# Performance work log

Hardware: AMD Instinct MI355X
Metric: run time of the kernel (lower is better)

Reference implementation:

```python
import jax, jax.numpy as jnp
import numpy as np

DECAY_CONSTANT = 1.0  # init kwarg decay_constant


def setup_inputs() -> dict:
    key = jax.random.key(0)
    k1, k2 = jax.random.split(key)
    B, E, S = 8, 1024, 2048
    x = jax.random.normal(k1, (B, E, S), dtype=jnp.float32)
    weight = jax.random.normal(k2, (1, S), dtype=jnp.float32)
    bias = jnp.zeros((S,), dtype=jnp.float32)
    decay_value = jnp.ones((1,), dtype=jnp.float32)
    return {"x": x, "weight": weight, "bias": bias, "decay_value": decay_value}


def _vector_to_matrix(v, decay_value):
    # v: (S,). M[i, j] = v[j] * clip(decay, 0.9, 1)^((j - i)/c) for j >= i, else 0.
    S = v.shape[0]
    i = jnp.arange(S)[:, None]
    j = jnp.arange(S)[None, :]
    d = jnp.clip(decay_value, 0.9, 1.0)  # shape (1,), broadcasts
    expo = (j - i).astype(v.dtype) / jnp.asarray(DECAY_CONSTANT, v.dtype)
    M = jnp.where(j >= i, v[None, :] * (d ** expo), jnp.zeros((), v.dtype))
    return M  # (S, S)


def reference(x, weight, bias, decay_value):
    # x: (B, E, S)
    v = weight.reshape(-1)
    W = _vector_to_matrix(v, decay_value).astype(x.dtype)
    out = jnp.einsum('bes,st->bet', x, W) + bias.astype(x.dtype)
    return out
```

## Files before the change

kernel.cpp:

```cpp
#include <hip/hip_runtime.h>


#define DECAY_CONSTANT 1.0f

__device__ __forceinline__ float readlane_f(float v, int l) {
    return __uint_as_float(__builtin_amdgcn_readlane(__float_as_uint(v), l));
}

__global__ __launch_bounds__(256) void decay_scan_kernel(
    const float* __restrict__ x,
    const float* __restrict__ weight,
    const float* __restrict__ bias,
    const float* __restrict__ decay,
    float* __restrict__ out,
    int nrows)
{
    constexpr int S  = 2048;
    constexpr int NC = 8;
    constexpr int CW = 256;

    const int lane = threadIdx.x & 63;
    const int wave = threadIdx.x >> 6;
    const int row  = blockIdx.x * 4 + wave;
    if (row >= nrows) return;

    float d = decay[0];
    d = fminf(fmaxf(d, 0.9f), 1.0f);
    const float r = (DECAY_CONSTANT == 1.0f) ? d : powf(d, 1.0f / DECAY_CONSTANT);

    const float r2 = r * r;
    const float r3 = r2 * r;
    const float r4 = r2 * r2;
    const float r8   = r4 * r4;
    const float r16  = r8 * r8;
    const float r32  = r16 * r16;
    const float r64  = r32 * r32;
    const float r128 = r64 * r64;
    const float r256 = r128 * r128;

    float r4L = 1.0f;
    r4L *= (lane & 1)  ? r4   : 1.0f;
    r4L *= (lane & 2)  ? r8   : 1.0f;
    r4L *= (lane & 4)  ? r16  : 1.0f;
    r4L *= (lane & 8)  ? r32  : 1.0f;
    r4L *= (lane & 16) ? r64  : 1.0f;
    r4L *= (lane & 32) ? r128 : 1.0f;

    const float* xr = x + (size_t)row * S;
    const int off4 = lane * 4;

    float4 p[NC], w[NC], bb[NC];
    #pragma unroll
    for (int c = 0; c < NC; ++c)
        p[c] = *reinterpret_cast<const float4*>(xr + c * CW + off4);
    #pragma unroll
    for (int c = 0; c < NC; ++c) {
        w[c]  = *reinterpret_cast<const float4*>(weight + c * CW + off4);
        bb[c] = *reinterpret_cast<const float4*>(bias   + c * CW + off4);
    }

    #pragma unroll
    for (int c = 0; c < NC; ++c) {
        p[c].y = fmaf(r, p[c].x, p[c].y);
        p[c].z = fmaf(r, p[c].y, p[c].z);
        p[c].w = fmaf(r, p[c].z, p[c].w);
    }

    float b[NC];
    #pragma unroll
    for (int c = 0; c < NC; ++c) b[c] = p[c].w;

    #pragma unroll
    for (int s = 0; s < 6; ++s) {
        const int off = 1 << s;
        const float m = (s == 0) ? r4 : (s == 1) ? r8 : (s == 2) ? r16
                      : (s == 3) ? r32 : (s == 4) ? r64 : r128;
        #pragma unroll
        for (int c = 0; c < NC; ++c) {
            float up = __shfl_up(b[c], off);
            if (lane >= off) b[c] = fmaf(m, up, b[c]);
        }
    }

    float t[NC], Tc[NC];
    #pragma unroll
    for (int c = 0; c < NC; ++c) {
        float bp = __shfl_up(b[c], 1);
        if (lane == 0) bp = 0.0f;
        t[c]  = bp;
        Tc[c] = readlane_f(b[c], 63);
    }

    float C = 0.0f;
    #pragma unroll
    for (int c = 0; c < NC; ++c) {
        t[c] = fmaf(C, r4L, t[c]);
        C = fmaf(r256, C, Tc[c]);
    }

    float* orow = out + (size_t)row * S;
    #pragma unroll
    for (int c = 0; c < NC; ++c) {
        float P0 = fmaf(r,  t[c], p[c].x);
        float P1 = fmaf(r2, t[c], p[c].y);
        float P2 = fmaf(r3, t[c], p[c].z);
        float P3 = fmaf(r4, t[c], p[c].w);
        float4 o;
        o.x = fmaf(w[c].x, P0, bb[c].x);
        o.y = fmaf(w[c].y, P1, bb[c].y);
        o.z = fmaf(w[c].z, P2, bb[c].z);
        o.w = fmaf(w[c].w, P3, bb[c].w);
        *reinterpret_cast<float4*>(orow + c * CW + off4) = o;
    }
}

extern "C" void kernel_launch(void* const* d_in, const int* in_sizes, int n_in,
                              void* d_out, int out_size, void* d_ws, size_t ws_size,
                              hipStream_t stream) {
    const float* x      = (const float*)d_in[0];
    const float* weight = (const float*)d_in[1];
    const float* bias   = (const float*)d_in[2];
    const float* decay  = (const float*)d_in[3];
    float* out = (float*)d_out;

    const int S = in_sizes[1];
    const int nrows = in_sizes[0] / S;

    const int blocks = (nrows + 3) / 4;
    decay_scan_kernel<<<blocks, 256, 0, stream>>>(x, weight, bias, decay, out, nrows);
}
```

Measured before the change: 25.20 us.

## Process four rows per wave with software-prefetched next-row loads

```diff
diff --git a/kernel.cpp b/kernel.cpp
--- a/kernel.cpp
+++ b/kernel.cpp
@@ -18,11 +18,12 @@
     constexpr int S  = 2048;
     constexpr int NC = 8;
     constexpr int CW = 256;
+    constexpr int RPW = 4;
 
-    const int lane = threadIdx.x & 63;
-    const int wave = threadIdx.x >> 6;
-    const int row  = blockIdx.x * 4 + wave;
-    if (row >= nrows) return;
+    const int lane   = threadIdx.x & 63;
+    const int wave   = threadIdx.x >> 6;
+    const int gw     = blockIdx.x * 4 + wave;
+    const int nwaves = gridDim.x * 4;
 
     float d = decay[0];
     d = fminf(fmaxf(d, 0.9f), 1.0f);
@@ -46,71 +47,98 @@
     r4L *= (lane & 16) ? r64  : 1.0f;
     r4L *= (lane & 32) ? r128 : 1.0f;
 
-    const float* xr = x + (size_t)row * S;
     const int off4 = lane * 4;
 
-    float4 p[NC], w[NC], bb[NC];
-    #pragma unroll
-    for (int c = 0; c < NC; ++c)
-        p[c] = *reinterpret_cast<const float4*>(xr + c * CW + off4);
+    float4 w[NC], bb[NC];
     #pragma unroll
     for (int c = 0; c < NC; ++c) {
         w[c]  = *reinterpret_cast<const float4*>(weight + c * CW + off4);
         bb[c] = *reinterpret_cast<const float4*>(bias   + c * CW + off4);
     }
 
-    #pragma unroll
-    for (int c = 0; c < NC; ++c) {
-        p[c].y = fmaf(r, p[c].x, p[c].y);
-        p[c].z = fmaf(r, p[c].y, p[c].z);
-        p[c].w = fmaf(r, p[c].z, p[c].w);
-    }
+    float4 pc[NC], pn[NC];
 
-    float b[NC];
-    #pragma unroll
-    for (int c = 0; c < NC; ++c) b[c] = p[c].w;
-
-    #pragma unroll
-    for (int s = 0; s < 6; ++s) {
-        const int off = 1 << s;
-        const float m = (s == 0) ? r4 : (s == 1) ? r8 : (s == 2) ? r16
-                      : (s == 3) ? r32 : (s == 4) ? r64 : r128;
-        #pragma unroll
-        for (int c = 0; c < NC; ++c) {
-            float up = __shfl_up(b[c], off);
-            if (lane >= off) b[c] = fmaf(m, up, b[c]);
+    {
+        const int row0 = gw;
+        if (row0 < nrows) {
+            const float* xr = x + (size_t)row0 * S;
+            #pragma unroll
+            for (int c = 0; c < NC; ++c)
+                pc[c] = *reinterpret_cast<const float4*>(xr + c * CW + off4);
         }
     }
 
-    float t[NC], Tc[NC];
     #pragma unroll
-    for (int c = 0; c < NC; ++c) {
-        float bp = __shfl_up(b[c], 1);
-        if (lane == 0) bp = 0.0f;
-        t[c]  = bp;
-        Tc[c] = readlane_f(b[c], 63);
-    }
+    for (int it = 0; it < RPW; ++it) {
+        const int row = gw + nwaves * it;
+        if (row >= nrows) break;
 
-    float C = 0.0f;
-    #pragma unroll
-    for (int c = 0; c < NC; ++c) {
-        t[c] = fmaf(C, r4L, t[c]);
-        C = fmaf(r256, C, Tc[c]);
-    }
+        const int nrow = row + nwaves;
+        if (it + 1 < RPW && nrow < nrows) {
+            const float* xr = x + (size_t)nrow * S;
+            #pragma unroll
+            for (int c = 0; c < NC; ++c)
+                pn[c] = *reinterpret_cast<const float4*>(xr + c * CW + off4);
+        }
 
-    float* orow = out + (size_t)row * S;
-    #pragma unroll
-    for (int c = 0; c < NC; ++c) {
-        float P0 = fmaf(r,  t[c], p[c].x);
-        float P1 = fmaf(r2, t[c], p[c].y);
-        float P2 = fmaf(r3, t[c], p[c].z);
-        float P3 = fmaf(r4, t[c], p[c].w);
-        float4 o;
-        o.x = fmaf(w[c].x, P0, bb[c].x);
-        o.y = fmaf(w[c].y, P1, bb[c].y);
-        o.z = fmaf(w[c].z, P2, bb[c].z);
-        o.w = fmaf(w[c].w, P3, bb[c].w);
-        *reinterpret_cast<float4*>(orow + c * CW + off4) = o;
+        float4 p[NC];
+        #pragma unroll
+        for (int c = 0; c < NC; ++c) {
+            p[c].x = pc[c].x;
+            p[c].y = fmaf(r, p[c].x, pc[c].y);
+            p[c].z = fmaf(r, p[c].y, pc[c].z);
+            p[c].w = fmaf(r, p[c].z, pc[c].w);
+        }
+
+        float b[NC];
+        #pragma unroll
+        for (int c = 0; c < NC; ++c) b[c] = p[c].w;
+
+        #pragma unroll
+        for (int s = 0; s < 6; ++s) {
+            const int off = 1 << s;
+            const float m = (s == 0) ? r4 : (s == 1) ? r8 : (s == 2) ? r16
+                          : (s == 3) ? r32 : (s == 4) ? r64 : r128;
+            #pragma unroll
+            for (int c = 0; c < NC; ++c) {
+                float up = __shfl_up(b[c], off);
+                if (lane >= off) b[c] = fmaf(m, up, b[c]);
+            }
+        }
+
+        float t[NC], Tc[NC];
+        #pragma unroll
+        for (int c = 0; c < NC; ++c) {
+            float bp = __shfl_up(b[c], 1);
+            if (lane == 0) bp = 0.0f;
+            t[c]  = bp;
+            Tc[c] = readlane_f(b[c], 63);
+        }
+
+        float C = 0.0f;
+        #pragma unroll
+        for (int c = 0; c < NC; ++c) {
+            t[c] = fmaf(C, r4L, t[c]);
+            C = fmaf(r256, C, Tc[c]);
+        }
+
+        float* orow = out + (size_t)row * S;
+        #pragma unroll
+        for (int c = 0; c < NC; ++c) {
+            float P0 = fmaf(r,  t[c], p[c].x);
+            float P1 = fmaf(r2, t[c], p[c].y);
+            float P2 = fmaf(r3, t[c], p[c].z);
+            float P3 = fmaf(r4, t[c], p[c].w);
+            float4 o;
+            o.x = fmaf(w[c].x, P0, bb[c].x);
+            o.y = fmaf(w[c].y, P1, bb[c].y);
+            o.z = fmaf(w[c].z, P2, bb[c].z);
+            o.w = fmaf(w[c].w, P3, bb[c].w);
+            *reinterpret_cast<float4*>(orow + c * CW + off4) = o;
+        }
+
+        #pragma unroll
+        for (int c = 0; c < NC; ++c) pc[c] = pn[c];
     }
 }
 
@@ -126,6 +154,7 @@
     const int S = in_sizes[1];
     const int nrows = in_sizes[0] / S;
 
-    const int blocks = (nrows + 3) / 4;
+    const int nwaves = (nrows + 3) / 4;
+    const int blocks = (nwaves + 3) / 4;
     decay_scan_kernel<<<blocks, 256, 0, stream>>>(x, weight, bias, decay, out, nrows);
 }
```

Measured after the change: 25.46 us. No clear change (+1.0%).
